# Performance work log

Measured on AMD Instinct MI355X. Metric: run time of the kernel, lower is better.

Reference implementation:

```python
import jax, jax.numpy as jnp
import numpy as np

N_NODES = 100000
N_RAND_EDGES = 1600000
EPS = 1e-12


def setup_inputs() -> dict:
    key = jax.random.key(0)
    k_x, k_w1, k_w2, k_r, k_c = jax.random.split(key, 5)
    X = jax.random.normal(k_x, (N_NODES, 256), dtype=jnp.float32)
    # Linear weights stored as [in, out] so forward is X @ W (bias=False)
    W1 = jax.random.normal(k_w1, (256, 128), dtype=jnp.float32) * 0.05
    W2 = jax.random.normal(k_w2, (128, 64), dtype=jnp.float32) * 0.05
    row = jax.random.randint(k_r, (N_RAND_EDGES,), 0, N_NODES, dtype=jnp.int32)
    col = jax.random.randint(k_c, (N_RAND_EDGES,), 0, N_NODES, dtype=jnp.int32)
    loops = jnp.arange(N_NODES, dtype=jnp.int32)  # self-loops (A has self-loops)
    edge_row = jnp.concatenate([row, loops])
    edge_col = jnp.concatenate([col, loops])
    return {"X": X, "W1": W1, "W2": W2, "edge_row": edge_row, "edge_col": edge_col}


def _norm_edge_weights(edge_row, edge_col):
    # degrees = row-sums of A (all values are 1.0)
    deg = jax.ops.segment_sum(jnp.ones_like(edge_row, dtype=jnp.float32), edge_row,
                              num_segments=N_NODES)
    d_inv_sqrt = 1.0 / jnp.clip(jnp.sqrt(deg), EPS)
    # A_hat = D^-1/2 A D^-1/2  <=>  per-edge weight
    return d_inv_sqrt[edge_row] * d_inv_sqrt[edge_col]


def _spmm(w, edge_row, edge_col, X):
    # (A_hat @ X)[i] = sum_{e: row_e = i} w_e * X[col_e]
    return jax.ops.segment_sum(w[:, None] * X[edge_col], edge_row,
                               num_segments=N_NODES)


def reference(X, W1, W2, edge_row, edge_col):
    w = _norm_edge_weights(edge_row, edge_col)
    # layer 0: GraphConvolution -> ReLU (dropout is identity in eval mode)
    H = jax.nn.relu(_spmm(w, edge_row, edge_col, X @ W1))
    # layer 1: GraphConvolution (logits)
    out = _spmm(w, edge_row, edge_col, H @ W2)
    return out
```

## Files before the change

### kernel.cpp

```cpp
#include <hip/hip_runtime.h>
#include <hip/hip_bf16.h>


typedef __attribute__((ext_vector_type(8))) short short8;
typedef __attribute__((ext_vector_type(4))) float floatx4;
typedef __attribute__((ext_vector_type(2))) float floatx2;

static __device__ __forceinline__ ushort f32_to_bf16_bits(float f) {
    union { ushort u; __hip_bfloat16 b; } cv;
    cv.b = __float2bfloat16(f);
    return cv.u;
}
static __device__ __forceinline__ float bf16lo_to_f32(uint u) {
    return __uint_as_float(u << 16);
}
static __device__ __forceinline__ float bf16hi_to_f32(uint u) {
    return __uint_as_float(u & 0xffff0000u);
}
static __device__ __forceinline__ uint pack2bf(float a, float b) {
    return (uint)f32_to_bf16_bits(a) | ((uint)f32_to_bf16_bits(b) << 16);
}

#define CSR_EPB 8192
#define SPMM_CHUNK 1024

__global__ __launch_bounds__(256) void scan_phase1_kernel(
    const int* __restrict__ in, int* __restrict__ out,
    int* __restrict__ block_total, int n) {
    __shared__ int tsum[256];
    int t = threadIdx.x;
    int base = blockIdx.x * 1024 + t * 4;
    int v0 = (base + 0 < n) ? in[base + 0] : 0;
    int v1 = (base + 1 < n) ? in[base + 1] : 0;
    int v2 = (base + 2 < n) ? in[base + 2] : 0;
    int v3 = (base + 3 < n) ? in[base + 3] : 0;
    tsum[t] = v0 + v1 + v2 + v3;
    __syncthreads();
    for (int off = 1; off < 256; off <<= 1) {
        int x = (t >= off) ? tsum[t - off] : 0;
        __syncthreads();
        tsum[t] += x;
        __syncthreads();
    }
    if (t == 255) block_total[blockIdx.x] = tsum[255];
    int run = (t == 0) ? 0 : tsum[t - 1];
    if (base + 0 < n) out[base + 0] = run; run += v0;
    if (base + 1 < n) out[base + 1] = run; run += v1;
    if (base + 2 < n) out[base + 2] = run; run += v2;
    if (base + 3 < n) out[base + 3] = run;
}

__global__ __launch_bounds__(256) void scan_phase2_kernel(
    const int* __restrict__ block_total, int* __restrict__ block_offset, int G) {
    __shared__ int s[256];
    int t = threadIdx.x;
    s[t] = (t < G) ? block_total[t] : 0;
    __syncthreads();
    for (int off = 1; off < 256; off <<= 1) {
        int x = (t >= off) ? s[t - off] : 0;
        __syncthreads();
        s[t] += x;
        __syncthreads();
    }
    if (t < G) block_offset[t] = (t == 0) ? 0 : s[t - 1];
    if (t == 0) block_offset[G] = s[255];
}

__global__ __launch_bounds__(256) void scan_phase3_kernel(
    int* __restrict__ arr, const int* __restrict__ block_offset, int n, int G) {
    int i = blockIdx.x * blockDim.x + threadIdx.x;
    if (i < n) arr[i] += block_offset[i >> 10];
    if (i == 0) arr[n] = block_offset[G];
}

__global__ __launch_bounds__(256) void edge_hist_cast_kernel(
    const int* __restrict__ keys, int* __restrict__ histG, int E, int nblk,
    const float* __restrict__ W1, const float* __restrict__ W2,
    ushort* __restrict__ W1t, ushort* __restrict__ W2t) {
    int b = blockIdx.x;
    if (b >= nblk) {
        int i = (b - nblk) * 256 + threadIdx.x;
        if (i < 256 * 128) {
            int n = i >> 8, k = i & 255;
            W1t[i] = f32_to_bf16_bits(W1[k * 128 + n]);
        } else {
            int j = i - 256 * 128;
            if (j < 128 * 64) {
                int n = j >> 7, k = j & 127;
                W2t[j] = f32_to_bf16_bits(W2[k * 64 + n]);
            }
        }
        return;
    }
    __shared__ int h[256];
    int t = threadIdx.x;
    h[t] = 0;
    __syncthreads();
    int base = b * CSR_EPB;
    int end = min(base + CSR_EPB, E);
    for (int i = base + t; i < end; i += 256)
        atomicAdd(&h[keys[i] >> 9], 1);
    __syncthreads();
    histG[t * nblk + b] = h[t];
}

__global__ __launch_bounds__(256) void edge_bin_kernel(
    const int* __restrict__ rows, const int* __restrict__ colsIn,
    const int* __restrict__ offG, const int* __restrict__ blk_off1,
    int* __restrict__ binP, int E, int nblk) {
    __shared__ int cur[256];
    int t = threadIdx.x;
    int idx = t * nblk + blockIdx.x;
    cur[t] = offG[idx] + blk_off1[idx >> 10];
    __syncthreads();
    int base = blockIdx.x * CSR_EPB;
    int end = min(base + CSR_EPB, E);
    for (int i = base + t; i < end; i += 256) {
        int r = rows[i], c = colsIn[i];
        int p = atomicAdd(&cur[r >> 9], 1);
        binP[p] = ((r & 511) << 17) | c;
    }
}

__global__ __launch_bounds__(256) void deg_dinv_from_bin_kernel(
    const int* __restrict__ binP, const int* __restrict__ offG,
    const int* __restrict__ blk_off1,
    int* __restrict__ deg, float* __restrict__ dinv, int E, int nblk, int N) {
    __shared__ int cnt[512];
    int b = blockIdx.x;
    int rbase = b << 9;
    if (rbase >= N) return;
    int t = threadIdx.x;
    for (int i = t; i < 512; i += 256) cnt[i] = 0;
    __syncthreads();
    int i0 = b * nblk;
    int bs = offG[i0] + blk_off1[i0 >> 10];
    int be = E;
    if (b + 1 < 256) {
        int i1 = (b + 1) * nblk;
        be = offG[i1] + blk_off1[i1 >> 10];
    }
    for (int e = bs + t; e < be; e += 256)
        atomicAdd(&cnt[binP[e] >> 17], 1);
    __syncthreads();
    for (int i = t; i < 512; i += 256) {
        int r = rbase + i;
        if (r < N) {
            int d = cnt[i];
            deg[r] = d;
            dinv[r] = 1.0f / sqrtf(fmaxf((float)d, 1e-24f));
        }
    }
}

__global__ __launch_bounds__(256) void edge_scatter_kernel(
    const int* __restrict__ binP, const int* __restrict__ offG,
    const int* __restrict__ blk_off1,
    const int* __restrict__ row_ptr, int* __restrict__ csr_col,
    int E, int nblk, int N) {
    __shared__ int cur[512];
    int b = blockIdx.x;
    int rbase = b << 9;
    if (rbase >= N) return;
    int t = threadIdx.x;
    for (int i = t; i < 512; i += 256) {
        int r = rbase + i;
        cur[i] = (r < N) ? row_ptr[r] : 0;
    }
    __syncthreads();
    int i0 = b * nblk;
    int bs = offG[i0] + blk_off1[i0 >> 10];
    int be = E;
    if (b + 1 < 256) {
        int i1 = (b + 1) * nblk;
        be = offG[i1] + blk_off1[i1 >> 10];
    }
    for (int e = bs + t; e < be; e += 256) {
        int pk = binP[e];
        int rl = pk >> 17;
        int c = pk & 0x1ffff;
        int p = atomicAdd(&cur[rl], 1);
        csr_col[p] = c;
    }
}

template <int KTOT, int NCOLS, bool AF32>
__global__ __launch_bounds__(256) void gemm_mfma_kernel(
    const void* __restrict__ Aptr, const ushort* __restrict__ Bt,
    const float* __restrict__ dinv, ushort* __restrict__ Cbf, int M) {
    constexpr int KP = 128;
    constexpr int COLT = NCOLS / 16;
    __shared__ ushort Bs[NCOLS][KP + 8];
    int tid = threadIdx.x;
    int wave = tid >> 6, lane = tid & 63;
    int quad = lane >> 4, l16 = lane & 15;
    int row0 = blockIdx.x * 64;
    int rowA = row0 + wave * 16 + l16;
    int rowAc = min(rowA, M - 1);

    floatx4 acc[COLT];
#pragma unroll
    for (int t = 0; t < COLT; t++) acc[t] = (floatx4){0.f, 0.f, 0.f, 0.f};

    for (int kp = 0; kp < KTOT; kp += KP) {
        for (int u = tid; u < NCOLS * (KP / 8); u += 256) {
            int n = u / (KP / 8);
            int k8 = (u % (KP / 8)) * 8;
            *(short8*)&Bs[n][k8] = *(const short8*)(Bt + (size_t)n * KTOT + kp + k8);
        }
        __syncthreads();
#pragma unroll
        for (int kc = 0; kc < KP / 32; kc++) {
            int kk = kp + kc * 32 + quad * 8;
            short8 a;
            if (AF32) {
                const float* ap = (const float*)Aptr + (size_t)rowAc * KTOT + kk;
                float4 f0 = *(const float4*)ap;
                float4 f1 = *(const float4*)(ap + 4);
                a[0] = (short)f32_to_bf16_bits(f0.x);
                a[1] = (short)f32_to_bf16_bits(f0.y);
                a[2] = (short)f32_to_bf16_bits(f0.z);
                a[3] = (short)f32_to_bf16_bits(f0.w);
                a[4] = (short)f32_to_bf16_bits(f1.x);
                a[5] = (short)f32_to_bf16_bits(f1.y);
                a[6] = (short)f32_to_bf16_bits(f1.z);
                a[7] = (short)f32_to_bf16_bits(f1.w);
            } else {
                a = *(const short8*)((const ushort*)Aptr + (size_t)rowAc * KTOT + kk);
            }
#pragma unroll
            for (int t = 0; t < COLT; t++) {
                short8 b = *(const short8*)&Bs[t * 16 + l16][kc * 32 + quad * 8];
                acc[t] = __builtin_amdgcn_mfma_f32_16x16x32_bf16(a, b, acc[t], 0, 0, 0);
            }
        }
        __syncthreads();
    }

#pragma unroll
    for (int r = 0; r < 4; r++) {
        int row = row0 + wave * 16 + quad * 4 + r;
        if (row < M) {
            float dv = dinv[row];
#pragma unroll
            for (int t = 0; t < COLT; t++)
                Cbf[(size_t)row * NCOLS + t * 16 + l16] = f32_to_bf16_bits(dv * acc[t][r]);
        }
    }
}

__global__ __launch_bounds__(256) void spmm_gemm2_kernel(
    const int* __restrict__ row_ptr, const int* __restrict__ cols,
    const float* __restrict__ dinv, const ushort* __restrict__ XW1,
    const ushort* __restrict__ W2t, ushort* __restrict__ HW2, int n) {
    __shared__ int cstage[SPMM_CHUNK];
    __shared__ ushort Hs[16][136];

    int tid = threadIdx.x;
    int wv = tid >> 6;
    int lane = tid & 63;
    int g = lane >> 4, lg = lane & 15;
    int r0 = blockIdx.x * 16;
    int row = r0 + wv * 4 + g;
    bool ok = row < n;
    int rc = ok ? row : (n - 1);
    int beg = row_ptr[rc];
    int end = ok ? row_ptr[rc + 1] : beg;
    int bbeg = row_ptr[r0];
    int bend = row_ptr[min(r0 + 16, n)];

    floatx2 acc2[4];
#pragma unroll
    for (int i = 0; i < 4; i++) acc2[i] = (floatx2){0.f, 0.f};

    const ushort* xb = XW1 + lg * 8;

#define ACC_DW(U, D)                                            \
    {                                                            \
        floatx2 v_;                                              \
        v_.x = bf16lo_to_f32(U);                                 \
        v_.y = bf16hi_to_f32(U);                                 \
        acc2[D] += v_;                                           \
    }
#define ACC_U4(UU)                                               \
    ACC_DW(UU.x, 0) ACC_DW(UU.y, 1) ACC_DW(UU.z, 2) ACC_DW(UU.w, 3)

    for (int cb = bbeg; cb < bend; cb += SPMM_CHUNK) {
        int ce = min(cb + SPMM_CHUNK, bend);
        __syncthreads();
        for (int i = cb + tid; i < ce; i += 256)
            cstage[i - cb] = cols[i];
        __syncthreads();
        int s = max(beg, cb), t_ = min(end, ce);
        int e = s;
        for (; e + 8 <= t_; e += 8) {
            int c0 = cstage[e - cb], c1 = cstage[e + 1 - cb];
            int c2 = cstage[e + 2 - cb], c3 = cstage[e + 3 - cb];
            int c4 = cstage[e + 4 - cb], c5 = cstage[e + 5 - cb];
            int c6 = cstage[e + 6 - cb], c7 = cstage[e + 7 - cb];
            uint4 u0 = *(const uint4*)(xb + (size_t)c0 * 128);
            uint4 u1 = *(const uint4*)(xb + (size_t)c1 * 128);
            uint4 u2 = *(const uint4*)(xb + (size_t)c2 * 128);
            uint4 u3 = *(const uint4*)(xb + (size_t)c3 * 128);
            uint4 u4 = *(const uint4*)(xb + (size_t)c4 * 128);
            uint4 u5 = *(const uint4*)(xb + (size_t)c5 * 128);
            uint4 u6 = *(const uint4*)(xb + (size_t)c6 * 128);
            uint4 u7 = *(const uint4*)(xb + (size_t)c7 * 128);
            ACC_U4(u0) ACC_U4(u1) ACC_U4(u2) ACC_U4(u3)
            ACC_U4(u4) ACC_U4(u5) ACC_U4(u6) ACC_U4(u7)
        }
        for (; e + 4 <= t_; e += 4) {
            int c0 = cstage[e - cb], c1 = cstage[e + 1 - cb];
            int c2 = cstage[e + 2 - cb], c3 = cstage[e + 3 - cb];
            uint4 u0 = *(const uint4*)(xb + (size_t)c0 * 128);
            uint4 u1 = *(const uint4*)(xb + (size_t)c1 * 128);
            uint4 u2 = *(const uint4*)(xb + (size_t)c2 * 128);
            uint4 u3 = *(const uint4*)(xb + (size_t)c3 * 128);
            ACC_U4(u0) ACC_U4(u1) ACC_U4(u2) ACC_U4(u3)
        }
        for (; e < t_; e++) {
            int c = cstage[e - cb];
            uint4 u = *(const uint4*)(xb + (size_t)c * 128);
            ACC_U4(u)
        }
    }
#undef ACC_U4
#undef ACC_DW

    {
        float dv = ok ? dinv[row] : 0.f;
        float a0 = fmaxf(dv * acc2[0].x, 0.f), a1 = fmaxf(dv * acc2[0].y, 0.f);
        float a2 = fmaxf(dv * acc2[1].x, 0.f), a3 = fmaxf(dv * acc2[1].y, 0.f);
        float a4 = fmaxf(dv * acc2[2].x, 0.f), a5 = fmaxf(dv * acc2[2].y, 0.f);
        float a6 = fmaxf(dv * acc2[3].x, 0.f), a7 = fmaxf(dv * acc2[3].y, 0.f);
        uint4 o;
        o.x = pack2bf(a0, a1);
        o.y = pack2bf(a2, a3);
        o.z = pack2bf(a4, a5);
        o.w = pack2bf(a6, a7);
        *(uint4*)&Hs[wv * 4 + g][lg * 8] = o;
    }
    __syncthreads();

    short8 bf[4];
#pragma unroll
    for (int kc = 0; kc < 4; kc++)
        bf[kc] = *(const short8*)(W2t + (wv * 16 + lg) * 128 + kc * 32 + g * 8);
    floatx4 dacc = (floatx4){0.f, 0.f, 0.f, 0.f};
#pragma unroll
    for (int kc = 0; kc < 4; kc++) {
        short8 a = *(const short8*)&Hs[lg][kc * 32 + g * 8];
        dacc = __builtin_amdgcn_mfma_f32_16x16x32_bf16(a, bf[kc], dacc, 0, 0, 0);
    }
#pragma unroll
    for (int r = 0; r < 4; r++) {
        int rowD = r0 + g * 4 + r;
        if (rowD < n)
            HW2[(size_t)rowD * 64 + wv * 16 + lg] =
                f32_to_bf16_bits(dinv[rowD] * dacc[r]);
    }
}

__global__ __launch_bounds__(256) void spmm_f64_kernel(
    const int* __restrict__ row_ptr, const int* __restrict__ cols,
    const float* __restrict__ dinv, const ushort* __restrict__ Xin,
    float* __restrict__ Yout, int n) {
    __shared__ int cstage[SPMM_CHUNK];
    int r0 = blockIdx.x * 32;
    int tid = threadIdx.x;
    int wv = tid >> 6;
    int lane = tid & 63;
    int h = lane >> 3, lh = lane & 7;
    int row = r0 + wv * 8 + h;
    bool ok = row < n;
    int rc = ok ? row : (n - 1);
    int beg = row_ptr[rc];
    int end = ok ? row_ptr[rc + 1] : beg;
    int bbeg = row_ptr[r0];
    int bend = row_ptr[min(r0 + 32, n)];

    floatx2 acc2[4];
#pragma unroll
    for (int i = 0; i < 4; i++) acc2[i] = (floatx2){0.f, 0.f};

    const ushort* xb = Xin + lh * 8;

#define ACC_DW(U, D)                                            \
    {                                                            \
        floatx2 v_;                                              \
        v_.x = bf16lo_to_f32(U);                                 \
        v_.y = bf16hi_to_f32(U);                                 \
        acc2[D] += v_;                                           \
    }
#define ACC_U4(UU)                                               \
    ACC_DW(UU.x, 0) ACC_DW(UU.y, 1) ACC_DW(UU.z, 2) ACC_DW(UU.w, 3)

    for (int cb = bbeg; cb < bend; cb += SPMM_CHUNK) {
        int ce = min(cb + SPMM_CHUNK, bend);
        __syncthreads();
        for (int i = cb + tid; i < ce; i += 256)
            cstage[i - cb] = cols[i];
        __syncthreads();
        int s = max(beg, cb), t_ = min(end, ce);
        int e = s;
        for (; e + 8 <= t_; e += 8) {
            int c0 = cstage[e - cb], c1 = cstage[e + 1 - cb];
            int c2 = cstage[e + 2 - cb], c3 = cstage[e + 3 - cb];
            int c4 = cstage[e + 4 - cb], c5 = cstage[e + 5 - cb];
            int c6 = cstage[e + 6 - cb], c7 = cstage[e + 7 - cb];
            uint4 u0 = *(const uint4*)(xb + (size_t)c0 * 64);
            uint4 u1 = *(const uint4*)(xb + (size_t)c1 * 64);
            uint4 u2 = *(const uint4*)(xb + (size_t)c2 * 64);
            uint4 u3 = *(const uint4*)(xb + (size_t)c3 * 64);
            uint4 u4 = *(const uint4*)(xb + (size_t)c4 * 64);
            uint4 u5 = *(const uint4*)(xb + (size_t)c5 * 64);
            uint4 u6 = *(const uint4*)(xb + (size_t)c6 * 64);
            uint4 u7 = *(const uint4*)(xb + (size_t)c7 * 64);
            ACC_U4(u0) ACC_U4(u1) ACC_U4(u2) ACC_U4(u3)
            ACC_U4(u4) ACC_U4(u5) ACC_U4(u6) ACC_U4(u7)
        }
        for (; e + 4 <= t_; e += 4) {
            int c0 = cstage[e - cb], c1 = cstage[e + 1 - cb];
            int c2 = cstage[e + 2 - cb], c3 = cstage[e + 3 - cb];
            uint4 u0 = *(const uint4*)(xb + (size_t)c0 * 64);
            uint4 u1 = *(const uint4*)(xb + (size_t)c1 * 64);
            uint4 u2 = *(const uint4*)(xb + (size_t)c2 * 64);
            uint4 u3 = *(const uint4*)(xb + (size_t)c3 * 64);
            ACC_U4(u0) ACC_U4(u1) ACC_U4(u2) ACC_U4(u3)
        }
        for (; e < t_; e++) {
            int c = cstage[e - cb];
            uint4 u = *(const uint4*)(xb + (size_t)c * 64);
            ACC_U4(u)
        }
    }
#undef ACC_U4
#undef ACC_DW

    if (ok) {
        float dv = dinv[row];
        float4 o0 = make_float4(dv * acc2[0].x, dv * acc2[0].y,
                                dv * acc2[1].x, dv * acc2[1].y);
        float4 o1 = make_float4(dv * acc2[2].x, dv * acc2[2].y,
                                dv * acc2[3].x, dv * acc2[3].y);
        float* yp = Yout + (size_t)row * 64 + lh * 8;
        *(float4*)yp = o0;
        *(float4*)(yp + 4) = o1;
    }
}


extern "C" void kernel_launch(void* const* d_in, const int* in_sizes, int n_in,
                              void* d_out, int out_size, void* d_ws, size_t ws_size,
                              hipStream_t stream) {
    const float* X  = (const float*)d_in[0];
    const float* W1 = (const float*)d_in[1];
    const float* W2 = (const float*)d_in[2];
    const int* erow = (const int*)d_in[3];
    const int* ecol = (const int*)d_in[4];

    const int N = in_sizes[0] / 256;
    const int E = in_sizes[3];
    const int G = (N + 1023) >> 10;

    const int nblk = (E + CSR_EPB - 1) / CSR_EPB;
    const int SL = 256 * nblk;
    const int GS = (SL + 1023) >> 10;
    const int GMAX = (G > GS) ? G : GS;
    const int CAST_BLKS = (256 * 128 + 128 * 64 + 255) / 256;

    char* ws = (char*)d_ws;
    size_t off = 0;
    auto carve = [&](size_t bytes) -> char* {
        char* p = ws + off;
        off += (bytes + 255) & ~(size_t)255;
        return p;
    };
    int*    deg       = (int*)   carve((size_t)N * 4);
    float*  dinv      = (float*) carve((size_t)N * 4);
    int*    row_ptr   = (int*)   carve((size_t)(N + 1) * 4);
    int*    blk_total = (int*)   carve((size_t)GMAX * 4);
    int*    blk_off1  = (int*)   carve((size_t)(GMAX + 1) * 4);
    int*    blk_off2  = (int*)   carve((size_t)(GMAX + 1) * 4);
    int*    offG      = (int*)   carve((size_t)(SL + 1) * 4);
    size_t binP_bytes = (size_t)E * 4;
    size_t xw1_bytes  = (size_t)N * 128 * 2;
    char*  uni        = carve(binP_bytes > xw1_bytes ? binP_bytes : xw1_bytes);
    int*    binP      = (int*)uni;
    ushort* XW1       = (ushort*)uni;
    int*    csr_col   = (int*)   carve((size_t)E * 4);
    ushort* W1t       = (ushort*)carve((size_t)256 * 128 * 2);
    ushort* W2t       = (ushort*)carve((size_t)128 * 64 * 2);
    ushort* HW2       = (ushort*)carve((size_t)N * 64 * 2);

    edge_hist_cast_kernel<<<nblk + CAST_BLKS, 256, 0, stream>>>(
        erow, offG, E, nblk, W1, W2, W1t, W2t);
    scan_phase1_kernel<<<GS, 256, 0, stream>>>(offG, offG, blk_total, SL);
    scan_phase2_kernel<<<1, 256, 0, stream>>>(blk_total, blk_off1, GS);
    edge_bin_kernel<<<nblk, 256, 0, stream>>>(erow, ecol, offG, blk_off1, binP, E, nblk);

    deg_dinv_from_bin_kernel<<<256, 256, 0, stream>>>(binP, offG, blk_off1, deg, dinv, E, nblk, N);
    scan_phase1_kernel<<<G, 256, 0, stream>>>(deg, row_ptr, blk_total, N);
    scan_phase2_kernel<<<1, 256, 0, stream>>>(blk_total, blk_off2, G);
    scan_phase3_kernel<<<(N + 255) / 256, 256, 0, stream>>>(row_ptr, blk_off2, N, G);

    edge_scatter_kernel<<<256, 256, 0, stream>>>(binP, offG, blk_off1, row_ptr, csr_col, E, nblk, N);

    gemm_mfma_kernel<256, 128, true><<<(N + 63) / 64, 256, 0, stream>>>(
        (const void*)X, W1t, dinv, XW1, N);

    spmm_gemm2_kernel<<<(N + 15) / 16, 256, 0, stream>>>(
        row_ptr, csr_col, dinv, XW1, W2t, HW2, N);

    spmm_f64_kernel<<<(N + 31) / 32, 256, 0, stream>>>(row_ptr, csr_col, dinv, HW2, (float*)d_out, N);
}
```

Measured before the change: 348.0 us.

## Drop LDS column staging and block barriers in SpMM kernels; per-wave MFMA epilogue

Both SpMM kernels stop staging column indices into shared memory in chunks guarded by __syncthreads and instead read cols directly from global memory per row. This removes the block-wide barriers that made waves wait for the slowest row in the block. In the fused gemm2 kernel, each wave now computes its own 4 rows of H@W2 with an LDS tile local to that wave, using only a waitcnt instead of a block barrier. The MFMA rows are mostly zero-padded (only 4 of 16 used), so matrix work goes up fourfold, and W2t is reloaded per wave.

Result: slower. 394.4 us (+13.4%).

```diff
diff --git a/kernel.cpp b/kernel.cpp
--- a/kernel.cpp
+++ b/kernel.cpp
@@ -22,7 +22,6 @@
 }
 
 #define CSR_EPB 8192
-#define SPMM_CHUNK 1024
 
 __global__ __launch_bounds__(256) void scan_phase1_kernel(
     const int* __restrict__ in, int* __restrict__ out,
@@ -253,8 +252,7 @@
     const int* __restrict__ row_ptr, const int* __restrict__ cols,
     const float* __restrict__ dinv, const ushort* __restrict__ XW1,
     const ushort* __restrict__ W2t, ushort* __restrict__ HW2, int n) {
-    __shared__ int cstage[SPMM_CHUNK];
-    __shared__ ushort Hs[16][136];
+    __shared__ ushort Hs[4][4][136];
 
     int tid = threadIdx.x;
     int wv = tid >> 6;
@@ -266,8 +264,6 @@
     int rc = ok ? row : (n - 1);
     int beg = row_ptr[rc];
     int end = ok ? row_ptr[rc + 1] : beg;
-    int bbeg = row_ptr[r0];
-    int bend = row_ptr[min(r0 + 16, n)];
 
     floatx2 acc2[4];
 #pragma unroll
@@ -285,44 +281,27 @@
 #define ACC_U4(UU)                                               \
     ACC_DW(UU.x, 0) ACC_DW(UU.y, 1) ACC_DW(UU.z, 2) ACC_DW(UU.w, 3)
 
-    for (int cb = bbeg; cb < bend; cb += SPMM_CHUNK) {
-        int ce = min(cb + SPMM_CHUNK, bend);
-        __syncthreads();
-        for (int i = cb + tid; i < ce; i += 256)
-            cstage[i - cb] = cols[i];
-        __syncthreads();
-        int s = max(beg, cb), t_ = min(end, ce);
-        int e = s;
-        for (; e + 8 <= t_; e += 8) {
-            int c0 = cstage[e - cb], c1 = cstage[e + 1 - cb];
-            int c2 = cstage[e + 2 - cb], c3 = cstage[e + 3 - cb];
-            int c4 = cstage[e + 4 - cb], c5 = cstage[e + 5 - cb];
-            int c6 = cstage[e + 6 - cb], c7 = cstage[e + 7 - cb];
-            uint4 u0 = *(const uint4*)(xb + (size_t)c0 * 128);
-            uint4 u1 = *(const uint4*)(xb + (size_t)c1 * 128);
-            uint4 u2 = *(const uint4*)(xb + (size_t)c2 * 128);
-            uint4 u3 = *(const uint4*)(xb + (size_t)c3 * 128);
-            uint4 u4 = *(const uint4*)(xb + (size_t)c4 * 128);
-            uint4 u5 = *(const uint4*)(xb + (size_t)c5 * 128);
-            uint4 u6 = *(const uint4*)(xb + (size_t)c6 * 128);
-            uint4 u7 = *(const uint4*)(xb + (size_t)c7 * 128);
-            ACC_U4(u0) ACC_U4(u1) ACC_U4(u2) ACC_U4(u3)
-            ACC_U4(u4) ACC_U4(u5) ACC_U4(u6) ACC_U4(u7)
-        }
-        for (; e + 4 <= t_; e += 4) {
-            int c0 = cstage[e - cb], c1 = cstage[e + 1 - cb];
-            int c2 = cstage[e + 2 - cb], c3 = cstage[e + 3 - cb];
-            uint4 u0 = *(const uint4*)(xb + (size_t)c0 * 128);
-            uint4 u1 = *(const uint4*)(xb + (size_t)c1 * 128);
-            uint4 u2 = *(const uint4*)(xb + (size_t)c2 * 128);
-            uint4 u3 = *(const uint4*)(xb + (size_t)c3 * 128);
-            ACC_U4(u0) ACC_U4(u1) ACC_U4(u2) ACC_U4(u3)
-        }
-        for (; e < t_; e++) {
-            int c = cstage[e - cb];
-            uint4 u = *(const uint4*)(xb + (size_t)c * 128);
-            ACC_U4(u)
-        }
+    int e = beg;
+    for (; e + 8 <= end; e += 8) {
+        int c0 = cols[e],     c1 = cols[e + 1];
+        int c2 = cols[e + 2], c3 = cols[e + 3];
+        int c4 = cols[e + 4], c5 = cols[e + 5];
+        int c6 = cols[e + 6], c7 = cols[e + 7];
+        uint4 u0 = *(const uint4*)(xb + (size_t)c0 * 128);
+        uint4 u1 = *(const uint4*)(xb + (size_t)c1 * 128);
+        uint4 u2 = *(const uint4*)(xb + (size_t)c2 * 128);
+        uint4 u3 = *(const uint4*)(xb + (size_t)c3 * 128);
+        uint4 u4 = *(const uint4*)(xb + (size_t)c4 * 128);
+        uint4 u5 = *(const uint4*)(xb + (size_t)c5 * 128);
+        uint4 u6 = *(const uint4*)(xb + (size_t)c6 * 128);
+        uint4 u7 = *(const uint4*)(xb + (size_t)c7 * 128);
+        ACC_U4(u0) ACC_U4(u1) ACC_U4(u2) ACC_U4(u3)
+        ACC_U4(u4) ACC_U4(u5) ACC_U4(u6) ACC_U4(u7)
+    }
+    for (; e < end; e++) {
+        int c = cols[e];
+        uint4 u = *(const uint4*)(xb + (size_t)c * 128);
+        ACC_U4(u)
     }
 #undef ACC_U4
 #undef ACC_DW
@@ -338,26 +317,35 @@
         o.y = pack2bf(a2, a3);
         o.z = pack2bf(a4, a5);
         o.w = pack2bf(a6, a7);
-        *(uint4*)&Hs[wv * 4 + g][lg * 8] = o;
-    }
-    __syncthreads();
-
-    short8 bf[4];
-#pragma unroll
-    for (int kc = 0; kc < 4; kc++)
-        bf[kc] = *(const short8*)(W2t + (wv * 16 + lg) * 128 + kc * 32 + g * 8);
-    floatx4 dacc = (floatx4){0.f, 0.f, 0.f, 0.f};
+        *(uint4*)&Hs[wv][g][lg * 8] = o;
+    }
+    asm volatile("s_waitcnt lgkmcnt(0)" ::: "memory");
+
+    floatx4 dacc[4];
+#pragma unroll
+    for (int t = 0; t < 4; t++) dacc[t] = (floatx4){0.f, 0.f, 0.f, 0.f};
 #pragma unroll
     for (int kc = 0; kc < 4; kc++) {
-        short8 a = *(const short8*)&Hs[lg][kc * 32 + g * 8];
-        dacc = __builtin_amdgcn_mfma_f32_16x16x32_bf16(a, bf[kc], dacc, 0, 0, 0);
-    }
-#pragma unroll
-    for (int r = 0; r < 4; r++) {
-        int rowD = r0 + g * 4 + r;
-        if (rowD < n)
-            HW2[(size_t)rowD * 64 + wv * 16 + lg] =
-                f32_to_bf16_bits(dinv[rowD] * dacc[r]);
+        short8 a = (short8){0, 0, 0, 0, 0, 0, 0, 0};
+        if (lg < 4) a = *(const short8*)&Hs[wv][lg][kc * 32 + g * 8];
+#pragma unroll
+        for (int t = 0; t < 4; t++) {
+            short8 b = *(const short8*)(W2t + (t * 16 + lg) * 128 + kc * 32 + g * 8);
+            dacc[t] = __builtin_amdgcn_mfma_f32_16x16x32_bf16(a, b, dacc[t], 0, 0, 0);
+        }
+    }
+    if (g == 0) {
+#pragma unroll
+        for (int r = 0; r < 4; r++) {
+            int rw = r0 + wv * 4 + r;
+            if (rw < n) {
+                float dv = dinv[rw];
+#pragma unroll
+                for (int t = 0; t < 4; t++)
+                    HW2[(size_t)rw * 64 + t * 16 + lg] =
+                        f32_to_bf16_bits(dv * dacc[t][r]);
+            }
+        }
     }
 }
 
@@ -365,19 +353,15 @@
     const int* __restrict__ row_ptr, const int* __restrict__ cols,
     const float* __restrict__ dinv, const ushort* __restrict__ Xin,
     float* __restrict__ Yout, int n) {
-    __shared__ int cstage[SPMM_CHUNK];
-    int r0 = blockIdx.x * 32;
     int tid = threadIdx.x;
     int wv = tid >> 6;
     int lane = tid & 63;
     int h = lane >> 3, lh = lane & 7;
-    int row = r0 + wv * 8 + h;
+    int row = blockIdx.x * 32 + wv * 8 + h;
     bool ok = row < n;
     int rc = ok ? row : (n - 1);
     int beg = row_ptr[rc];
     int end = ok ? row_ptr[rc + 1] : beg;
-    int bbeg = row_ptr[r0];
-    int bend = row_ptr[min(r0 + 32, n)];
 
     floatx2 acc2[4];
 #pragma unroll
@@ -395,44 +379,27 @@
 #define ACC_U4(UU)                                               \
     ACC_DW(UU.x, 0) ACC_DW(UU.y, 1) ACC_DW(UU.z, 2) ACC_DW(UU.w, 3)
 
-    for (int cb = bbeg; cb < bend; cb += SPMM_CHUNK) {
-        int ce = min(cb + SPMM_CHUNK, bend);
-        __syncthreads();
-        for (int i = cb + tid; i < ce; i += 256)
-            cstage[i - cb] = cols[i];
-        __syncthreads();
-        int s = max(beg, cb), t_ = min(end, ce);
-        int e = s;
-        for (; e + 8 <= t_; e += 8) {
-            int c0 = cstage[e - cb], c1 = cstage[e + 1 - cb];
-            int c2 = cstage[e + 2 - cb], c3 = cstage[e + 3 - cb];
-            int c4 = cstage[e + 4 - cb], c5 = cstage[e + 5 - cb];
-            int c6 = cstage[e + 6 - cb], c7 = cstage[e + 7 - cb];
-            uint4 u0 = *(const uint4*)(xb + (size_t)c0 * 64);
-            uint4 u1 = *(const uint4*)(xb + (size_t)c1 * 64);
-            uint4 u2 = *(const uint4*)(xb + (size_t)c2 * 64);
-            uint4 u3 = *(const uint4*)(xb + (size_t)c3 * 64);
-            uint4 u4 = *(const uint4*)(xb + (size_t)c4 * 64);
-            uint4 u5 = *(const uint4*)(xb + (size_t)c5 * 64);
-            uint4 u6 = *(const uint4*)(xb + (size_t)c6 * 64);
-            uint4 u7 = *(const uint4*)(xb + (size_t)c7 * 64);
-            ACC_U4(u0) ACC_U4(u1) ACC_U4(u2) ACC_U4(u3)
-            ACC_U4(u4) ACC_U4(u5) ACC_U4(u6) ACC_U4(u7)
-        }
-        for (; e + 4 <= t_; e += 4) {
-            int c0 = cstage[e - cb], c1 = cstage[e + 1 - cb];
-            int c2 = cstage[e + 2 - cb], c3 = cstage[e + 3 - cb];
-            uint4 u0 = *(const uint4*)(xb + (size_t)c0 * 64);
-            uint4 u1 = *(const uint4*)(xb + (size_t)c1 * 64);
-            uint4 u2 = *(const uint4*)(xb + (size_t)c2 * 64);
-            uint4 u3 = *(const uint4*)(xb + (size_t)c3 * 64);
-            ACC_U4(u0) ACC_U4(u1) ACC_U4(u2) ACC_U4(u3)
-        }
-        for (; e < t_; e++) {
-            int c = cstage[e - cb];
-            uint4 u = *(const uint4*)(xb + (size_t)c * 64);
-            ACC_U4(u)
-        }
+    int e = beg;
+    for (; e + 8 <= end; e += 8) {
+        int c0 = cols[e],     c1 = cols[e + 1];
+        int c2 = cols[e + 2], c3 = cols[e + 3];
+        int c4 = cols[e + 4], c5 = cols[e + 5];
+        int c6 = cols[e + 6], c7 = cols[e + 7];
+        uint4 u0 = *(const uint4*)(xb + (size_t)c0 * 64);
+        uint4 u1 = *(const uint4*)(xb + (size_t)c1 * 64);
+        uint4 u2 = *(const uint4*)(xb + (size_t)c2 * 64);
+        uint4 u3 = *(const uint4*)(xb + (size_t)c3 * 64);
+        uint4 u4 = *(const uint4*)(xb + (size_t)c4 * 64);
+        uint4 u5 = *(const uint4*)(xb + (size_t)c5 * 64);
+        uint4 u6 = *(const uint4*)(xb + (size_t)c6 * 64);
+        uint4 u7 = *(const uint4*)(xb + (size_t)c7 * 64);
+        ACC_U4(u0) ACC_U4(u1) ACC_U4(u2) ACC_U4(u3)
+        ACC_U4(u4) ACC_U4(u5) ACC_U4(u6) ACC_U4(u7)
+    }
+    for (; e < end; e++) {
+        int c = cols[e];
+        uint4 u = *(const uint4*)(xb + (size_t)c * 64);
+        ACC_U4(u)
     }
 #undef ACC_U4
 #undef ACC_DW
```

## Fuse CSR build pipeline into single cooperative kernel with grid syncs

Applied to the files above, without the earlier changes.

Replaces nine small launches (histogram, scans, binning, degree, scatter) with one cooperative kernel of 256 blocks that uses grid.sync between phases. This removes per-launch overhead and the idle gaps between dependent kernels. In exchange, every phase is limited to 256 blocks, so the histogram and binning phases (about 208 chunks) and the W cast lose parallelism, and each grid-wide barrier has its own cost.

New measurement: 586.4 us. +68.5%, slower.

```diff
diff --git a/kernel.cpp b/kernel.cpp
--- a/kernel.cpp
+++ b/kernel.cpp
@@ -1,5 +1,8 @@
 #include <hip/hip_runtime.h>
 #include <hip/hip_bf16.h>
+#include <hip/hip_cooperative_groups.h>
+
+namespace cg = cooperative_groups;
 
 
 typedef __attribute__((ext_vector_type(8))) short short8;
@@ -24,12 +27,11 @@
 #define CSR_EPB 8192
 #define SPMM_CHUNK 1024
 
-__global__ __launch_bounds__(256) void scan_phase1_kernel(
-    const int* __restrict__ in, int* __restrict__ out,
-    int* __restrict__ block_total, int n) {
-    __shared__ int tsum[256];
+
+static __device__ void scan1024_block(const int* in, int* out, int* block_total,
+                                      int n, int vb, int* tsum) {
     int t = threadIdx.x;
-    int base = blockIdx.x * 1024 + t * 4;
+    int base = vb * 1024 + t * 4;
     int v0 = (base + 0 < n) ? in[base + 0] : 0;
     int v1 = (base + 1 < n) ? in[base + 1] : 0;
     int v2 = (base + 2 < n) ? in[base + 2] : 0;
@@ -42,19 +44,19 @@
         tsum[t] += x;
         __syncthreads();
     }
-    if (t == 255) block_total[blockIdx.x] = tsum[255];
+    if (t == 255) block_total[vb] = tsum[255];
     int run = (t == 0) ? 0 : tsum[t - 1];
     if (base + 0 < n) out[base + 0] = run; run += v0;
     if (base + 1 < n) out[base + 1] = run; run += v1;
     if (base + 2 < n) out[base + 2] = run; run += v2;
     if (base + 3 < n) out[base + 3] = run;
-}
-
-__global__ __launch_bounds__(256) void scan_phase2_kernel(
-    const int* __restrict__ block_total, int* __restrict__ block_offset, int G) {
-    __shared__ int s[256];
+    __syncthreads();
+}
+
+static __device__ void scan_small_block(const int* block_total, int* block_offset,
+                                        int Gn, int* s) {
     int t = threadIdx.x;
-    s[t] = (t < G) ? block_total[t] : 0;
+    s[t] = (t < Gn) ? block_total[t] : 0;
     __syncthreads();
     for (int off = 1; off < 256; off <<= 1) {
         int x = (t >= off) ? s[t - off] : 0;
@@ -62,125 +64,129 @@
         s[t] += x;
         __syncthreads();
     }
-    if (t < G) block_offset[t] = (t == 0) ? 0 : s[t - 1];
-    if (t == 0) block_offset[G] = s[255];
-}
-
-__global__ __launch_bounds__(256) void scan_phase3_kernel(
-    int* __restrict__ arr, const int* __restrict__ block_offset, int n, int G) {
-    int i = blockIdx.x * blockDim.x + threadIdx.x;
-    if (i < n) arr[i] += block_offset[i >> 10];
-    if (i == 0) arr[n] = block_offset[G];
-}
-
-__global__ __launch_bounds__(256) void edge_hist_cast_kernel(
-    const int* __restrict__ keys, int* __restrict__ histG, int E, int nblk,
+    if (t < Gn) block_offset[t] = (t == 0) ? 0 : s[t - 1];
+    if (t == 0) block_offset[Gn] = s[255];
+    __syncthreads();
+}
+
+__global__ __launch_bounds__(256) void csr_build_coop_kernel(
+    const int* __restrict__ erow, const int* __restrict__ ecol,
     const float* __restrict__ W1, const float* __restrict__ W2,
-    ushort* __restrict__ W1t, ushort* __restrict__ W2t) {
-    int b = blockIdx.x;
-    if (b >= nblk) {
-        int i = (b - nblk) * 256 + threadIdx.x;
+    ushort* __restrict__ W1t, ushort* __restrict__ W2t,
+    int* __restrict__ offG, int* __restrict__ blk_total,
+    int* __restrict__ blk_off1, int* __restrict__ blk_off2,
+    int* __restrict__ binP, int* __restrict__ deg, float* __restrict__ dinv,
+    int* __restrict__ row_ptr, int* __restrict__ csr_col,
+    int E, int N, int nblk, int SL, int GS, int G) {
+    cg::grid_group grid = cg::this_grid();
+    __shared__ int sh[512];
+    int t = threadIdx.x;
+    int B = gridDim.x;
+
+    for (int b = blockIdx.x; b < nblk; b += B) {
+        sh[t] = 0;
+        __syncthreads();
+        int base = b * CSR_EPB, end = min(base + CSR_EPB, E);
+        for (int i = base + t; i < end; i += 256)
+            atomicAdd(&sh[erow[i] >> 9], 1);
+        __syncthreads();
+        offG[t * nblk + b] = sh[t];
+        __syncthreads();
+    }
+    for (int i = blockIdx.x * 256 + t; i < 256 * 128 + 128 * 64; i += B * 256) {
         if (i < 256 * 128) {
             int n = i >> 8, k = i & 255;
             W1t[i] = f32_to_bf16_bits(W1[k * 128 + n]);
         } else {
             int j = i - 256 * 128;
-            if (j < 128 * 64) {
-                int n = j >> 7, k = j & 127;
-                W2t[j] = f32_to_bf16_bits(W2[k * 64 + n]);
-            }
-        }
-        return;
-    }
-    __shared__ int h[256];
-    int t = threadIdx.x;
-    h[t] = 0;
-    __syncthreads();
-    int base = b * CSR_EPB;
-    int end = min(base + CSR_EPB, E);
-    for (int i = base + t; i < end; i += 256)
-        atomicAdd(&h[keys[i] >> 9], 1);
-    __syncthreads();
-    histG[t * nblk + b] = h[t];
-}
-
-__global__ __launch_bounds__(256) void edge_bin_kernel(
-    const int* __restrict__ rows, const int* __restrict__ colsIn,
-    const int* __restrict__ offG, const int* __restrict__ blk_off1,
-    int* __restrict__ binP, int E, int nblk) {
-    __shared__ int cur[256];
-    int t = threadIdx.x;
-    int idx = t * nblk + blockIdx.x;
-    cur[t] = offG[idx] + blk_off1[idx >> 10];
-    __syncthreads();
-    int base = blockIdx.x * CSR_EPB;
-    int end = min(base + CSR_EPB, E);
-    for (int i = base + t; i < end; i += 256) {
-        int r = rows[i], c = colsIn[i];
-        int p = atomicAdd(&cur[r >> 9], 1);
-        binP[p] = ((r & 511) << 17) | c;
-    }
-}
-
-__global__ __launch_bounds__(256) void deg_dinv_from_bin_kernel(
-    const int* __restrict__ binP, const int* __restrict__ offG,
-    const int* __restrict__ blk_off1,
-    int* __restrict__ deg, float* __restrict__ dinv, int E, int nblk, int N) {
-    __shared__ int cnt[512];
-    int b = blockIdx.x;
-    int rbase = b << 9;
-    if (rbase >= N) return;
-    int t = threadIdx.x;
-    for (int i = t; i < 512; i += 256) cnt[i] = 0;
-    __syncthreads();
-    int i0 = b * nblk;
-    int bs = offG[i0] + blk_off1[i0 >> 10];
-    int be = E;
-    if (b + 1 < 256) {
-        int i1 = (b + 1) * nblk;
-        be = offG[i1] + blk_off1[i1 >> 10];
-    }
-    for (int e = bs + t; e < be; e += 256)
-        atomicAdd(&cnt[binP[e] >> 17], 1);
-    __syncthreads();
-    for (int i = t; i < 512; i += 256) {
-        int r = rbase + i;
-        if (r < N) {
-            int d = cnt[i];
-            deg[r] = d;
-            dinv[r] = 1.0f / sqrtf(fmaxf((float)d, 1e-24f));
-        }
-    }
-}
-
-__global__ __launch_bounds__(256) void edge_scatter_kernel(
-    const int* __restrict__ binP, const int* __restrict__ offG,
-    const int* __restrict__ blk_off1,
-    const int* __restrict__ row_ptr, int* __restrict__ csr_col,
-    int E, int nblk, int N) {
-    __shared__ int cur[512];
-    int b = blockIdx.x;
-    int rbase = b << 9;
-    if (rbase >= N) return;
-    int t = threadIdx.x;
-    for (int i = t; i < 512; i += 256) {
-        int r = rbase + i;
-        cur[i] = (r < N) ? row_ptr[r] : 0;
-    }
-    __syncthreads();
-    int i0 = b * nblk;
-    int bs = offG[i0] + blk_off1[i0 >> 10];
-    int be = E;
-    if (b + 1 < 256) {
-        int i1 = (b + 1) * nblk;
-        be = offG[i1] + blk_off1[i1 >> 10];
-    }
-    for (int e = bs + t; e < be; e += 256) {
-        int pk = binP[e];
-        int rl = pk >> 17;
-        int c = pk & 0x1ffff;
-        int p = atomicAdd(&cur[rl], 1);
-        csr_col[p] = c;
+            int n = j >> 7, k = j & 127;
+            W2t[j] = f32_to_bf16_bits(W2[k * 64 + n]);
+        }
+    }
+    grid.sync();
+
+    for (int vb = blockIdx.x; vb < GS; vb += B)
+        scan1024_block(offG, offG, blk_total, SL, vb, sh);
+    grid.sync();
+    if (blockIdx.x == 0) scan_small_block(blk_total, blk_off1, GS, sh);
+    grid.sync();
+
+    for (int b = blockIdx.x; b < nblk; b += B) {
+        int idx = t * nblk + b;
+        sh[t] = offG[idx] + blk_off1[idx >> 10];
+        __syncthreads();
+        int base = b * CSR_EPB, end = min(base + CSR_EPB, E);
+        for (int i = base + t; i < end; i += 256) {
+            int r = erow[i], c = ecol[i];
+            int p = atomicAdd(&sh[r >> 9], 1);
+            binP[p] = ((r & 511) << 17) | c;
+        }
+        __syncthreads();
+    }
+    grid.sync();
+
+    for (int b = blockIdx.x; b < 256; b += B) {
+        int rbase = b << 9;
+        if (rbase < N) {
+            for (int i = t; i < 512; i += 256) sh[i] = 0;
+            __syncthreads();
+            int i0 = b * nblk;
+            int bs = offG[i0] + blk_off1[i0 >> 10];
+            int be = E;
+            if (b + 1 < 256) {
+                int i1 = (b + 1) * nblk;
+                be = offG[i1] + blk_off1[i1 >> 10];
+            }
+            for (int e = bs + t; e < be; e += 256)
+                atomicAdd(&sh[binP[e] >> 17], 1);
+            __syncthreads();
+            for (int i = t; i < 512; i += 256) {
+                int r = rbase + i;
+                if (r < N) {
+                    int d = sh[i];
+                    deg[r] = d;
+                    dinv[r] = 1.0f / sqrtf(fmaxf((float)d, 1e-24f));
+                }
+            }
+            __syncthreads();
+        }
+    }
+    grid.sync();
+
+    for (int vb = blockIdx.x; vb < G; vb += B)
+        scan1024_block(deg, row_ptr, blk_total, N, vb, sh);
+    grid.sync();
+    if (blockIdx.x == 0) scan_small_block(blk_total, blk_off2, G, sh);
+    grid.sync();
+    for (int i = blockIdx.x * 256 + t; i < N; i += B * 256)
+        row_ptr[i] += blk_off2[i >> 10];
+    if (blockIdx.x == 0 && t == 0) row_ptr[N] = blk_off2[G];
+    grid.sync();
+
+    for (int b = blockIdx.x; b < 256; b += B) {
+        int rbase = b << 9;
+        if (rbase < N) {
+            for (int i = t; i < 512; i += 256) {
+                int r = rbase + i;
+                sh[i] = (r < N) ? row_ptr[r] : 0;
+            }
+            __syncthreads();
+            int i0 = b * nblk;
+            int bs = offG[i0] + blk_off1[i0 >> 10];
+            int be = E;
+            if (b + 1 < 256) {
+                int i1 = (b + 1) * nblk;
+                be = offG[i1] + blk_off1[i1 >> 10];
+            }
+            for (int e = bs + t; e < be; e += 256) {
+                int pk = binP[e];
+                int rl = pk >> 17;
+                int c = pk & 0x1ffff;
+                int p = atomicAdd(&sh[rl], 1);
+                csr_col[p] = c;
+            }
+            __syncthreads();
+        }
     }
 }
 
@@ -467,7 +473,6 @@
     const int SL = 256 * nblk;
     const int GS = (SL + 1023) >> 10;
     const int GMAX = (G > GS) ? G : GS;
-    const int CAST_BLKS = (256 * 128 + 128 * 64 + 255) / 256;
 
     char* ws = (char*)d_ws;
     size_t off = 0;
@@ -493,18 +498,25 @@
     ushort* W2t       = (ushort*)carve((size_t)128 * 64 * 2);
     ushort* HW2       = (ushort*)carve((size_t)N * 64 * 2);
 
-    edge_hist_cast_kernel<<<nblk + CAST_BLKS, 256, 0, stream>>>(
-        erow, offG, E, nblk, W1, W2, W1t, W2t);
-    scan_phase1_kernel<<<GS, 256, 0, stream>>>(offG, offG, blk_total, SL);
-    scan_phase2_kernel<<<1, 256, 0, stream>>>(blk_total, blk_off1, GS);
-    edge_bin_kernel<<<nblk, 256, 0, stream>>>(erow, ecol, offG, blk_off1, binP, E, nblk);
-
-    deg_dinv_from_bin_kernel<<<256, 256, 0, stream>>>(binP, offG, blk_off1, deg, dinv, E, nblk, N);
-    scan_phase1_kernel<<<G, 256, 0, stream>>>(deg, row_ptr, blk_total, N);
-    scan_phase2_kernel<<<1, 256, 0, stream>>>(blk_total, blk_off2, G);
-    scan_phase3_kernel<<<(N + 255) / 256, 256, 0, stream>>>(row_ptr, blk_off2, N, G);
-
-    edge_scatter_kernel<<<256, 256, 0, stream>>>(binP, offG, blk_off1, row_ptr, csr_col, E, nblk, N);
+    {
+        const int* erow_ = erow; const int* ecol_ = ecol;
+        const float* W1_ = W1; const float* W2_ = W2;
+        ushort* W1t_ = W1t; ushort* W2t_ = W2t;
+        int* offG_ = offG; int* blk_total_ = blk_total;
+        int* blk_off1_ = blk_off1; int* blk_off2_ = blk_off2;
+        int* binP_ = binP; int* deg_ = deg; float* dinv_ = dinv;
+        int* row_ptr_ = row_ptr; int* csr_col_ = csr_col;
+        int E_ = E, N_ = N, nblk_ = nblk, SL_ = SL, GS_ = GS, G_ = G;
+        void* args[] = {
+            (void*)&erow_, (void*)&ecol_, (void*)&W1_, (void*)&W2_,
+            (void*)&W1t_, (void*)&W2t_, (void*)&offG_, (void*)&blk_total_,
+            (void*)&blk_off1_, (void*)&blk_off2_, (void*)&binP_, (void*)&deg_,
+            (void*)&dinv_, (void*)&row_ptr_, (void*)&csr_col_,
+            (void*)&E_, (void*)&N_, (void*)&nblk_, (void*)&SL_, (void*)&GS_,
+            (void*)&G_};
+        hipLaunchCooperativeKernel((const void*)csr_build_coop_kernel,
+                                   dim3(256), dim3(256), args, 0, stream);
+    }
 
     gemm_mfma_kernel<256, 128, true><<<(N + 63) / 64, 256, 0, stream>>>(
         (const void*)X, W1t, dinv, XW1, N);
```
